# Optimization experiments

Hardware: AMD Instinct MI355X
Metric: run time of the kernel (lower is better)

## Reference

```python
import jax, jax.numpy as jnp
import numpy as np

EPS = 1e-5
OUTPUT_BINS = 1000


def _act_quant(x):
    # per-token absmax int8 quantization (BitNet b1.58)
    scale = 127.0 / jnp.clip(jnp.max(jnp.abs(x), axis=-1, keepdims=True), EPS, None)
    return jnp.clip(jnp.round(x * scale), -128.0, 127.0) / scale


def _weight_quant(w):
    # ternary absmean quantization
    scale = 1.0 / jnp.clip(jnp.mean(jnp.abs(w)), EPS, None)
    return jnp.clip(jnp.round(w * scale), -1.0, 1.0) / scale


def _ste(x, q):
    return x + jax.lax.stop_gradient(q - x)


def bitlinear(x, w):
    xq = _ste(x, _act_quant(x))
    wq = _ste(w, _weight_quant(w))
    return jnp.einsum('bi,oi->bo', xq, wq)


def layernorm(x, g, b):
    mu = jnp.mean(x, axis=-1, keepdims=True)
    var = jnp.mean(jnp.square(x - mu), axis=-1, keepdims=True)
    return (x - mu) * jax.lax.rsqrt(var + EPS) * g + b


def setup_inputs() -> dict:
    key = jax.random.key(0)
    ks = jax.random.split(key, 5)
    B, D_IN, H = 4096, 1024, 4096
    return {
        'x': jax.random.normal(ks[0], (B, D_IN), dtype=jnp.float32),
        'W0': jax.random.normal(ks[1], (H, D_IN), dtype=jnp.float32) * 0.02,
        'W1': jax.random.normal(ks[2], (H, H), dtype=jnp.float32) * 0.02,
        'W2': jax.random.normal(ks[3], (H, H), dtype=jnp.float32) * 0.02,
        'W3': jax.random.normal(ks[4], (2 * OUTPUT_BINS, H), dtype=jnp.float32) * 0.02,
        'g0': jnp.ones((H,), jnp.float32), 'b0': jnp.zeros((H,), jnp.float32),
        'g1': jnp.ones((H,), jnp.float32), 'b1': jnp.zeros((H,), jnp.float32),
        'g2': jnp.ones((H,), jnp.float32), 'b2': jnp.zeros((H,), jnp.float32),
    }


def reference(x, W0, W1, W2, W3, g0, b0, g1, b1, g2, b2):
    h = jax.nn.silu(layernorm(bitlinear(x, W0), g0, b0))
    h = jax.nn.silu(layernorm(bitlinear(h, W1), g1, b1))
    h = jax.nn.silu(layernorm(bitlinear(h, W2), g2, b2))
    out = bitlinear(h, W3)                      # [B, 2*output_bins]
    mz_logits, int_logits = jnp.split(out, 2, axis=-1)
    mz_values = jax.nn.sigmoid(mz_logits) * (OUTPUT_BINS - 1) + 1.0
    intensities = jax.nn.sigmoid(int_logits) * 100.0
    return (mz_values, intensities)
```

## Files before the change

kernel.cpp:

```cpp
#include <hip/hip_runtime.h>
#include <hip/hip_bf16.h>
#include <cstdint>
#include <cstddef>

#define EPS 1e-5f

typedef __attribute__((ext_vector_type(4))) int int32x4;

__device__ __forceinline__ float blk_sum(float v, float* s4) {
    #pragma unroll
    for (int o = 32; o; o >>= 1) v += __shfl_down(v, o, 64);
    if ((threadIdx.x & 63) == 0) s4[threadIdx.x >> 6] = v;
    __syncthreads();
    v = s4[0] + s4[1] + s4[2] + s4[3];
    __syncthreads();
    return v;
}

__device__ __forceinline__ void blk_sum2(float& a, float& b, float* s8) {
    #pragma unroll
    for (int o = 32; o; o >>= 1) {
        a += __shfl_down(a, o, 64);
        b += __shfl_down(b, o, 64);
    }
    if ((threadIdx.x & 63) == 0) {
        s8[threadIdx.x >> 6] = a;
        s8[4 + (threadIdx.x >> 6)] = b;
    }
    __syncthreads();
    a = s8[0] + s8[1] + s8[2] + s8[3];
    b = s8[4] + s8[5] + s8[6] + s8[7];
    __syncthreads();
}

__device__ __forceinline__ float blk_max(float v, float* s4) {
    #pragma unroll
    for (int o = 32; o; o >>= 1) v = fmaxf(v, __shfl_down(v, o, 64));
    if ((threadIdx.x & 63) == 0) s4[threadIdx.x >> 6] = v;
    __syncthreads();
    v = fmaxf(fmaxf(s4[0], s4[1]), fmaxf(s4[2], s4[3]));
    __syncthreads();
    return v;
}

__device__ __forceinline__ int pack4(float a, float b, float c, float d, float lo, float hi) {
    int x0 = (int)fminf(fmaxf(a, lo), hi);
    int x1 = (int)fminf(fmaxf(b, lo), hi);
    int x2 = (int)fminf(fmaxf(c, lo), hi);
    int x3 = (int)fminf(fmaxf(d, lo), hi);
    return (x0 & 255) | ((x1 & 255) << 8) | ((x2 & 255) << 16) | ((x3 & 255) << 24);
}

__device__ __forceinline__ float bflo(unsigned u) { return __uint_as_float(u << 16); }
__device__ __forceinline__ float bfhi(unsigned u) { return __uint_as_float(u & 0xffff0000u); }

__global__ __launch_bounds__(256) void absmean_all_kernel(
    const float* __restrict__ W0, const float* __restrict__ W1,
    const float* __restrict__ W2, const float* __restrict__ W3,
    float* __restrict__ part) {
    __shared__ float s4[4];
    const float* w; int sidx; unsigned rel;
    unsigned bx = blockIdx.x;
    if (bx < 1024)      { w = W0; sidx = 0; rel = bx; }
    else if (bx < 5120) { w = W1; sidx = 1; rel = bx - 1024; }
    else if (bx < 9216) { w = W2; sidx = 2; rel = bx - 5120; }
    else                { w = W3; sidx = 3; rel = bx - 9216; }
    const float4* p = (const float4*)w + (size_t)rel * 1024 + threadIdx.x;
    float4 v0 = p[0], v1 = p[256], v2 = p[512], v3 = p[768];
    float s = fabsf(v0.x) + fabsf(v0.y) + fabsf(v0.z) + fabsf(v0.w)
            + fabsf(v1.x) + fabsf(v1.y) + fabsf(v1.z) + fabsf(v1.w)
            + fabsf(v2.x) + fabsf(v2.y) + fabsf(v2.z) + fabsf(v2.w)
            + fabsf(v3.x) + fabsf(v3.y) + fabsf(v3.z) + fabsf(v3.w);
    s = blk_sum(s, s4);
    if (threadIdx.x == 0) atomicAdd(&part[(sidx * 64 + (rel & 63)) * 16], s);
}

__global__ __launch_bounds__(256) void reduce_sums_kernel(const float* __restrict__ part,
                                                          float* __restrict__ sums) {
    int w = threadIdx.x >> 6, l = threadIdx.x & 63;
    float v = part[(w * 64 + l) * 16];
    #pragma unroll
    for (int o = 32; o; o >>= 1) v += __shfl_down(v, o, 64);
    if (l == 0) sums[w] = v;
}

__global__ __launch_bounds__(256) void wquant_all_kernel(
    const float* __restrict__ W0, const float* __restrict__ W1,
    const float* __restrict__ W2, const float* __restrict__ W3,
    int* __restrict__ q0, int* __restrict__ q1, int* __restrict__ q2, int* __restrict__ q3,
    const float* __restrict__ sums) {
    const float* w; int* q; int sidx; unsigned rel; float invN; bool pad = false;
    unsigned bx = blockIdx.x;
    if (bx < 1024)      { w = W0; q = q0; sidx = 0; rel = bx;        invN = 1.f / 4194304.f; }
    else if (bx < 5120) { w = W1; q = q1; sidx = 1; rel = bx - 1024; invN = 1.f / 16777216.f; }
    else if (bx < 9216) { w = W2; q = q2; sidx = 2; rel = bx - 5120; invN = 1.f / 16777216.f; }
    else                { w = W3; q = q3; sidx = 3; rel = bx - 9216; invN = 1.f / 8192000.f;
                          pad = (rel >= 2000); }
    int4 o = {0, 0, 0, 0};
    if (!pad) {
        float mean = fmaxf(sums[sidx] * invN, EPS);
        float scale = 1.f / mean;
        const float4* p = (const float4*)w + (size_t)rel * 1024 + threadIdx.x * 4;
        float4 v0 = p[0], v1 = p[1], v2 = p[2], v3 = p[3];
        o.x = pack4(rintf(v0.x * scale), rintf(v0.y * scale), rintf(v0.z * scale), rintf(v0.w * scale), -1.f, 1.f);
        o.y = pack4(rintf(v1.x * scale), rintf(v1.y * scale), rintf(v1.z * scale), rintf(v1.w * scale), -1.f, 1.f);
        o.z = pack4(rintf(v2.x * scale), rintf(v2.y * scale), rintf(v2.z * scale), rintf(v2.w * scale), -1.f, 1.f);
        o.w = pack4(rintf(v3.x * scale), rintf(v3.y * scale), rintf(v3.z * scale), rintf(v3.w * scale), -1.f, 1.f);
    }
    ((int4*)q)[(size_t)rel * 256 + threadIdx.x] = o;
}

__global__ __launch_bounds__(256) void actquant_kernel(const float* __restrict__ x,
                                                       int* __restrict__ q,
                                                       float* __restrict__ inv_s) {
    __shared__ float s4[4];
    int row = blockIdx.x;
    const float4* xr = (const float4*)(x + (size_t)row * 1024);
    float4 v = xr[threadIdx.x];
    float m = fmaxf(fmaxf(fabsf(v.x), fabsf(v.y)), fmaxf(fabsf(v.z), fabsf(v.w)));
    m = blk_max(m, s4);
    m = fmaxf(m, EPS);
    float scale = 127.f / m;
    if (threadIdx.x == 0) inv_s[row] = m / 127.f;
    q[(size_t)row * 256 + threadIdx.x] =
        pack4(rintf(v.x * scale), rintf(v.y * scale),
              rintf(v.z * scale), rintf(v.w * scale), -128.f, 127.f);
}

__global__ __launch_bounds__(256) void ln_silu_quant_kernel(const ushort* __restrict__ h,
                                                            const float* __restrict__ g,
                                                            const float* __restrict__ b,
                                                            int* __restrict__ q,
                                                            float* __restrict__ inv_s) {
    __shared__ float s8[8];
    int row = blockIdx.x;
    int t = threadIdx.x;
    const uint4* hr = (const uint4*)(h + (size_t)row * 4096);
    uint4 p0 = hr[t * 2], p1 = hr[t * 2 + 1];
    float f[16];
    f[0] = bflo(p0.x); f[1] = bfhi(p0.x); f[2] = bflo(p0.y); f[3] = bfhi(p0.y);
    f[4] = bflo(p0.z); f[5] = bfhi(p0.z); f[6] = bflo(p0.w); f[7] = bfhi(p0.w);
    f[8] = bflo(p1.x); f[9] = bfhi(p1.x); f[10] = bflo(p1.y); f[11] = bfhi(p1.y);
    f[12] = bflo(p1.z); f[13] = bfhi(p1.z); f[14] = bflo(p1.w); f[15] = bfhi(p1.w);
    float sum = 0.f, sq = 0.f;
    #pragma unroll
    for (int i = 0; i < 16; i++) { sum += f[i]; sq += f[i] * f[i]; }
    blk_sum2(sum, sq, s8);
    float mu = sum * (1.f / 4096.f);
    float var = sq * (1.f / 4096.f) - mu * mu;
    float rs = rsqrtf(var + EPS);
    const float4* g4 = (const float4*)g;
    const float4* b4 = (const float4*)b;
    float amax = 0.f;
    #pragma unroll
    for (int i = 0; i < 4; i++) {
        float4 gg = g4[t * 4 + i];
        float4 bb = b4[t * 4 + i];
        float y0 = (f[i * 4 + 0] - mu) * rs * gg.x + bb.x;
        float y1 = (f[i * 4 + 1] - mu) * rs * gg.y + bb.y;
        float y2 = (f[i * 4 + 2] - mu) * rs * gg.z + bb.z;
        float y3 = (f[i * 4 + 3] - mu) * rs * gg.w + bb.w;
        f[i * 4 + 0] = y0 / (1.f + expf(-y0));
        f[i * 4 + 1] = y1 / (1.f + expf(-y1));
        f[i * 4 + 2] = y2 / (1.f + expf(-y2));
        f[i * 4 + 3] = y3 / (1.f + expf(-y3));
    }
    #pragma unroll
    for (int i = 0; i < 16; i++) amax = fmaxf(amax, fabsf(f[i]));
    amax = blk_max(amax, s8);
    amax = fmaxf(amax, EPS);
    float scale = 127.f / amax;
    if (t == 0) inv_s[row] = amax / 127.f;
    int4 o;
    o.x = pack4(rintf(f[0] * scale), rintf(f[1] * scale), rintf(f[2] * scale), rintf(f[3] * scale), -128.f, 127.f);
    o.y = pack4(rintf(f[4] * scale), rintf(f[5] * scale), rintf(f[6] * scale), rintf(f[7] * scale), -128.f, 127.f);
    o.z = pack4(rintf(f[8] * scale), rintf(f[9] * scale), rintf(f[10] * scale), rintf(f[11] * scale), -128.f, 127.f);
    o.w = pack4(rintf(f[12] * scale), rintf(f[13] * scale), rintf(f[14] * scale), rintf(f[15] * scale), -128.f, 127.f);
    ((int4*)((char*)q + (size_t)row * 4096))[t] = o;
}

__device__ __forceinline__ void load_lds16(const void* g, void* l) {
    __builtin_amdgcn_global_load_lds((__attribute__((address_space(1))) void*)(g),
                                     (__attribute__((address_space(3))) void*)(l), 16, 0, 0);
}

template <int MODE>
__global__ __launch_bounds__(256, 2) void gemm_i8_kernel(
    const char* __restrict__ A, const char* __restrict__ B,
    const float* __restrict__ inv_s, const float* __restrict__ wsum, float invWN,
    int K, void* __restrict__ outp) {
    __shared__ __align__(16) char lA[128 * 128];
    __shared__ __align__(16) char lB[128 * 128];
    const int t = threadIdx.x;
    const int lane = t & 63;
    const int wave = t >> 6;
    const int bm = blockIdx.y * 128, bn = blockIdx.x * 128;
    const int wr = (wave >> 1) * 64, wc = (wave & 1) * 64;

    int32x4 acc[4][4] = {};

    const int r0 = t >> 3;
    const int c0 = (t & 7) * 16;
    const int gcol = c0 ^ (16 * (r0 & 7));
    const char* gA = A + (size_t)(bm + r0) * K + gcol;
    const char* gB = B + (size_t)(bn + r0) * K + gcol;
    char* sA = lA + t * 16;
    char* sB = lB + t * 16;

    const int fr = lane & 15;
    const int fq = lane >> 4;
    const int swz = 16 * (fr & 7);

    for (int k0 = 0; k0 < K; k0 += 128) {
        #pragma unroll
        for (int j = 0; j < 4; j++)
            load_lds16(gA + (size_t)(j * 32) * K + k0, sA + j * 4096);
        #pragma unroll
        for (int j = 0; j < 4; j++)
            load_lds16(gB + (size_t)(j * 32) * K + k0, sB + j * 4096);
        __syncthreads();

        #pragma unroll
        for (int ks = 0; ks < 2; ks++) {
            const int col = (ks * 64 + fq * 16) ^ swz;
            int32x4 af[4], bf[4];
            #pragma unroll
            for (int mt = 0; mt < 4; mt++)
                af[mt] = *(const int32x4*)(lA + (wr + mt * 16 + fr) * 128 + col);
            #pragma unroll
            for (int nt = 0; nt < 4; nt++)
                bf[nt] = *(const int32x4*)(lB + (wc + nt * 16 + fr) * 128 + col);
            #pragma unroll
            for (int mt = 0; mt < 4; mt++) {
                #pragma unroll
                for (int nt = 0; nt < 4; nt++) {
                    acc[mt][nt] = __builtin_amdgcn_mfma_i32_16x16x64_i8(af[mt], bf[nt],
                                                                        acc[mt][nt], 0, 0, 0);
                }
            }
        }
        __syncthreads();
    }

    const float wmean = fmaxf(wsum[0] * invWN, EPS);
    #pragma unroll
    for (int mt = 0; mt < 4; mt++) {
        #pragma unroll
        for (int rg = 0; rg < 4; rg++) {
            int gr = bm + wr + mt * 16 + fq * 4 + rg;
            float rowscale = inv_s[gr] * wmean;
            #pragma unroll
            for (int nt = 0; nt < 4; nt++) {
                int gc = bn + wc + nt * 16 + fr;
                float v = (float)acc[mt][nt][rg] * rowscale;
                if (MODE == 0) {
                    ((__hip_bfloat16*)outp)[(size_t)gr * 4096 + gc] = __float2bfloat16(v);
                } else {
                    if (gc < 2000) {
                        float sg = 1.f / (1.f + expf(-v));
                        float* out = (float*)outp;
                        if (gc < 1000)
                            out[(size_t)gr * 1000 + gc] = sg * 999.f + 1.f;
                        else
                            out[(size_t)4096 * 1000 + (size_t)gr * 1000 + (gc - 1000)] =
                                sg * 100.f;
                    }
                }
            }
        }
    }
}

template <int MH>
__device__ __forceinline__ void mfma_quad(int32x4 (&acc)[8][4], const int32x4 (&af)[4],
                                          const int32x4 (&bf)[4]) {
    #pragma unroll
    for (int i = 0; i < 4; i++) {
        #pragma unroll
        for (int j = 0; j < 4; j++) {
            acc[MH * 4 + i][j] =
                __builtin_amdgcn_mfma_i32_16x16x64_i8(af[i], bf[j], acc[MH * 4 + i][j], 0, 0, 0);
        }
    }
}

__global__ __launch_bounds__(512, 2) void gemm_i8_pipe(
    const char* __restrict__ A, const char* __restrict__ B,
    const float* __restrict__ inv_s, const float* __restrict__ wsum, float invWN,
    int K, __hip_bfloat16* __restrict__ outp) {
    __shared__ __align__(16) char lA[4][256][64];
    __shared__ __align__(16) char lB[4][256][64];
    const int t = threadIdx.x;
    const int lane = t & 63;
    const int wave = t >> 6;

    const int nwg = gridDim.x * gridDim.y;
    const int wg0 = blockIdx.y * gridDim.x + blockIdx.x;
    const int q8 = nwg >> 3;
    const int wg = (wg0 & 7) * q8 + (wg0 >> 3);
    const int bm = (wg / gridDim.x) * 256;
    const int bn = (wg % gridDim.x) * 256;

    const int wr = (wave >> 2) * 128;
    const int wc = (wave & 3) * 64;
    const int fr = lane & 15;
    const int fq = lane >> 4;

    const int srow = t >> 2;
    const int schunk = ((t & 3) ^ ((t >> 3) & 3)) * 16;
    const char* gA = A + (size_t)(bm + srow) * K + schunk;
    const char* gB = B + (size_t)(bn + srow) * K + schunk;
    char* sAd = &lA[0][0][0] + t * 16;
    char* sBd = &lB[0][0][0] + t * 16;

    const int rchunk = (fq ^ ((fr >> 1) & 3)) * 16;
    const char* aRd = &lA[0][0][0] + (wr + fr) * 64 + rchunk;
    const char* bRd = &lB[0][0][0] + (wc + fr) * 64 + rchunk;

    int32x4 acc[8][4] = {};
    int32x4 afX[4], afY[4], bfX[4], bfY[4];
    const int NT = K >> 6;

#define STAGE_A(buf, kt) { \
    load_lds16(gA + (size_t)(kt) * 64, sAd + (buf) * 16384); \
    load_lds16(gA + (size_t)128 * K + (size_t)(kt) * 64, sAd + (buf) * 16384 + 8192); }
#define STAGE_B(buf, kt) { \
    load_lds16(gB + (size_t)(kt) * 64, sBd + (buf) * 16384); \
    load_lds16(gB + (size_t)128 * K + (size_t)(kt) * 64, sBd + (buf) * 16384 + 8192); }
#define LD_AF(dst, buf, mh) { \
    const char* p_ = aRd + (buf) * 16384 + (mh) * 4096; \
    dst[0] = *(const int32x4*)(p_); \
    dst[1] = *(const int32x4*)(p_ + 1024); \
    dst[2] = *(const int32x4*)(p_ + 2048); \
    dst[3] = *(const int32x4*)(p_ + 3072); }
#define LD_BF(dst, buf) { \
    const char* p_ = bRd + (buf) * 16384; \
    dst[0] = *(const int32x4*)(p_); \
    dst[1] = *(const int32x4*)(p_ + 1024); \
    dst[2] = *(const int32x4*)(p_ + 2048); \
    dst[3] = *(const int32x4*)(p_ + 3072); }
#define WAITL(n) { asm volatile("s_waitcnt lgkmcnt(" #n ")" ::: "memory"); \
                   __builtin_amdgcn_sched_barrier(0); }
#define WAITV(n) { asm volatile("s_waitcnt vmcnt(" #n ")" ::: "memory"); \
                   __builtin_amdgcn_sched_barrier(0); }
#define BAR() { __builtin_amdgcn_s_barrier(); __builtin_amdgcn_sched_barrier(0); }
#define MF0(afc, bfc) { __builtin_amdgcn_s_setprio(1); mfma_quad<0>(acc, afc, bfc); \
                        __builtin_amdgcn_s_setprio(0); }
#define MF1(afc, bfc) { __builtin_amdgcn_s_setprio(1); mfma_quad<1>(acc, afc, bfc); \
                        __builtin_amdgcn_s_setprio(0); }

    STAGE_A(0, 0); STAGE_B(0, 0);
    STAGE_A(1, 1); STAGE_B(1, 1);
    STAGE_A(2, 2); STAGE_B(2, 2);
    WAITV(8);
    BAR();
    LD_BF(bfX, 0); LD_AF(afX, 0, 0);

    for (int kt = 0; kt <= NT - 8; kt += 4) {
        STAGE_A(3, kt + 3); LD_AF(afY, 0, 1); WAITL(4); MF0(afX, bfX); WAITV(6); BAR();
        STAGE_B(3, kt + 3); LD_BF(bfY, 1); LD_AF(afX, 1, 0); WAITL(8); MF1(afY, bfX); BAR();
        STAGE_A(0, kt + 4); LD_AF(afY, 1, 1); WAITL(4); MF0(afX, bfY); WAITV(6); BAR();
        STAGE_B(0, kt + 4); LD_BF(bfX, 2); LD_AF(afX, 2, 0); WAITL(8); MF1(afY, bfY); BAR();
        STAGE_A(1, kt + 5); LD_AF(afY, 2, 1); WAITL(4); MF0(afX, bfX); WAITV(6); BAR();
        STAGE_B(1, kt + 5); LD_BF(bfY, 3); LD_AF(afX, 3, 0); WAITL(8); MF1(afY, bfX); BAR();
        STAGE_A(2, kt + 6); LD_AF(afY, 3, 1); WAITL(4); MF0(afX, bfY); WAITV(6); BAR();
        STAGE_B(2, kt + 6); LD_BF(bfX, 0); LD_AF(afX, 0, 0); WAITL(8); MF1(afY, bfY); BAR();
    }

    STAGE_A(3, NT - 1); LD_AF(afY, 0, 1); WAITL(4); MF0(afX, bfX); WAITV(6); BAR();
    STAGE_B(3, NT - 1); LD_BF(bfY, 1); LD_AF(afX, 1, 0); WAITL(8); MF1(afY, bfX); BAR();
    LD_AF(afY, 1, 1); WAITL(4); MF0(afX, bfY); WAITV(4); BAR();
    LD_BF(bfX, 2); LD_AF(afX, 2, 0); WAITL(8); MF1(afY, bfY); BAR();
    LD_AF(afY, 2, 1); WAITL(4); MF0(afX, bfX); WAITV(0); BAR();
    LD_BF(bfY, 3); LD_AF(afX, 3, 0); WAITL(8); MF1(afY, bfX); BAR();
    LD_AF(afY, 3, 1); WAITL(4); MF0(afX, bfY); BAR();
    WAITL(0); MF1(afY, bfY);

#undef STAGE_A
#undef STAGE_B
#undef LD_AF
#undef LD_BF
#undef WAITL
#undef WAITV
#undef BAR
#undef MF0
#undef MF1

    const float wmean = fmaxf(wsum[0] * invWN, EPS);
    #pragma unroll
    for (int mt = 0; mt < 8; mt++) {
        #pragma unroll
        for (int rg = 0; rg < 4; rg++) {
            const int gr = bm + wr + mt * 16 + fq * 4 + rg;
            const float rowscale = inv_s[gr] * wmean;
            #pragma unroll
            for (int nt = 0; nt < 4; nt++) {
                const int gc = bn + wc + nt * 16 + fr;
                outp[(size_t)gr * 4096 + gc] =
                    __float2bfloat16((float)acc[mt][nt][rg] * rowscale);
            }
        }
    }
}

extern "C" void kernel_launch(void* const* d_in, const int* in_sizes, int n_in,
                              void* d_out, int out_size, void* d_ws, size_t ws_size,
                              hipStream_t stream) {
    const float* x  = (const float*)d_in[0];
    const float* W0 = (const float*)d_in[1];
    const float* W1 = (const float*)d_in[2];
    const float* W2 = (const float*)d_in[3];
    const float* W3 = (const float*)d_in[4];
    const float* g0 = (const float*)d_in[5];
    const float* b0 = (const float*)d_in[6];
    const float* g1 = (const float*)d_in[7];
    const float* b1 = (const float*)d_in[8];
    const float* g2 = (const float*)d_in[9];
    const float* b2 = (const float*)d_in[10];
    float* out = (float*)d_out;

    char* ws = (char*)d_ws;
    size_t off = 0;
    auto alloc = [&](size_t bytes) -> char* {
        char* p = ws + off;
        off = (off + bytes + 255) & ~(size_t)255;
        return p;
    };
    float* part = (float*)alloc(256 * 16 * sizeof(float));
    float* sums = (float*)alloc(4 * sizeof(float));
    float* inv0 = (float*)alloc(4096 * 4);
    float* inv1 = (float*)alloc(4096 * 4);
    float* inv2 = (float*)alloc(4096 * 4);
    float* inv3 = (float*)alloc(4096 * 4);
    char* wq0 = alloc(4096ll * 1024);
    char* wq1 = alloc(4096ll * 4096);
    char* wq2 = alloc(4096ll * 4096);
    char* wq3 = alloc(2048ll * 4096);
    char* a0  = alloc(4096ll * 1024);
    char* a1  = alloc(4096ll * 4096);
    char* a2  = alloc(4096ll * 4096);
    char* h   = alloc(4096ll * 4096 * 2);
    char* a3 = a1;

    hipMemsetAsync(part, 0, 256 * 16 * sizeof(float), stream);

    absmean_all_kernel<<<11216, 256, 0, stream>>>(W0, W1, W2, W3, part);
    reduce_sums_kernel<<<1, 256, 0, stream>>>(part, sums);
    actquant_kernel<<<4096, 256, 0, stream>>>(x, (int*)a0, inv0);
    wquant_all_kernel<<<11264, 256, 0, stream>>>(W0, W1, W2, W3, (int*)wq0, (int*)wq1,
                                                 (int*)wq2, (int*)wq3, sums);

    gemm_i8_pipe<<<dim3(16, 16), 512, 0, stream>>>(a0, wq0, inv0, sums + 0,
                                                   1.f / 4194304.f, 1024,
                                                   (__hip_bfloat16*)h);
    ln_silu_quant_kernel<<<4096, 256, 0, stream>>>((const ushort*)h, g0, b0, (int*)a1, inv1);

    gemm_i8_pipe<<<dim3(16, 16), 512, 0, stream>>>(a1, wq1, inv1, sums + 1,
                                                   1.f / 16777216.f, 4096,
                                                   (__hip_bfloat16*)h);
    ln_silu_quant_kernel<<<4096, 256, 0, stream>>>((const ushort*)h, g1, b1, (int*)a2, inv2);

    gemm_i8_pipe<<<dim3(16, 16), 512, 0, stream>>>(a2, wq2, inv2, sums + 2,
                                                   1.f / 16777216.f, 4096,
                                                   (__hip_bfloat16*)h);
    ln_silu_quant_kernel<<<4096, 256, 0, stream>>>((const ushort*)h, g2, b2, (int*)a3, inv3);

    gemm_i8_kernel<1><<<dim3(16, 32), 256, 0, stream>>>(a3, wq3, inv3, sums + 3,
                                                        1.f / 8192000.f, 4096, out);
}
```

Baseline: 515.4 us.

## Restructure int8 GEMM pipeline to full-tile register double buffering per k-step

Replaces the half-tile ping-pong schedule, with two barriers per k-tile, by one that loads all 8 A fragments and 4 B fragments per k-tile into double-buffered registers. Both A and B global stages are issued together, so there is one barrier per k-tile instead of two. Launch bounds drop to one workgroup per SIMD group to make room for the larger fragment register set. This cuts synchronisation overhead but lowers occupancy and makes the LDS-read and MFMA overlap coarser.

```diff
diff --git a/kernel.cpp b/kernel.cpp
--- a/kernel.cpp
+++ b/kernel.cpp
@@ -271,20 +271,19 @@
     }
 }
 
-template <int MH>
-__device__ __forceinline__ void mfma_quad(int32x4 (&acc)[8][4], const int32x4 (&af)[4],
-                                          const int32x4 (&bf)[4]) {
-    #pragma unroll
-    for (int i = 0; i < 4; i++) {
+__device__ __forceinline__ void mfma_32(int32x4 (&acc)[8][4], const int32x4 (&af)[8],
+                                        const int32x4 (&bf)[4]) {
+    #pragma unroll
+    for (int i = 0; i < 8; i++) {
         #pragma unroll
         for (int j = 0; j < 4; j++) {
-            acc[MH * 4 + i][j] =
-                __builtin_amdgcn_mfma_i32_16x16x64_i8(af[i], bf[j], acc[MH * 4 + i][j], 0, 0, 0);
+            acc[i][j] =
+                __builtin_amdgcn_mfma_i32_16x16x64_i8(af[i], bf[j], acc[i][j], 0, 0, 0);
         }
     }
 }
 
-__global__ __launch_bounds__(512, 2) void gemm_i8_pipe(
+__global__ __launch_bounds__(512, 1) void gemm_i8_pipe(
     const char* __restrict__ A, const char* __restrict__ B,
     const float* __restrict__ inv_s, const float* __restrict__ wsum, float invWN,
     int K, __hip_bfloat16* __restrict__ outp) {
@@ -318,7 +317,7 @@
     const char* bRd = &lB[0][0][0] + (wc + fr) * 64 + rchunk;
 
     int32x4 acc[8][4] = {};
-    int32x4 afX[4], afY[4], bfX[4], bfY[4];
+    int32x4 aX[8], aY[8], bX[4], bY[4];
     const int NT = K >> 6;
 
 #define STAGE_A(buf, kt) { \
@@ -327,13 +326,17 @@
 #define STAGE_B(buf, kt) { \
     load_lds16(gB + (size_t)(kt) * 64, sBd + (buf) * 16384); \
     load_lds16(gB + (size_t)128 * K + (size_t)(kt) * 64, sBd + (buf) * 16384 + 8192); }
-#define LD_AF(dst, buf, mh) { \
-    const char* p_ = aRd + (buf) * 16384 + (mh) * 4096; \
+#define LD_A8(dst, buf) { \
+    const char* p_ = aRd + (buf) * 16384; \
     dst[0] = *(const int32x4*)(p_); \
     dst[1] = *(const int32x4*)(p_ + 1024); \
     dst[2] = *(const int32x4*)(p_ + 2048); \
-    dst[3] = *(const int32x4*)(p_ + 3072); }
-#define LD_BF(dst, buf) { \
+    dst[3] = *(const int32x4*)(p_ + 3072); \
+    dst[4] = *(const int32x4*)(p_ + 4096); \
+    dst[5] = *(const int32x4*)(p_ + 5120); \
+    dst[6] = *(const int32x4*)(p_ + 6144); \
+    dst[7] = *(const int32x4*)(p_ + 7168); }
+#define LD_B4(dst, buf) { \
     const char* p_ = bRd + (buf) * 16384; \
     dst[0] = *(const int32x4*)(p_); \
     dst[1] = *(const int32x4*)(p_ + 1024); \
@@ -344,47 +347,48 @@
 #define WAITV(n) { asm volatile("s_waitcnt vmcnt(" #n ")" ::: "memory"); \
                    __builtin_amdgcn_sched_barrier(0); }
 #define BAR() { __builtin_amdgcn_s_barrier(); __builtin_amdgcn_sched_barrier(0); }
-#define MF0(afc, bfc) { __builtin_amdgcn_s_setprio(1); mfma_quad<0>(acc, afc, bfc); \
-                        __builtin_amdgcn_s_setprio(0); }
-#define MF1(afc, bfc) { __builtin_amdgcn_s_setprio(1); mfma_quad<1>(acc, afc, bfc); \
-                        __builtin_amdgcn_s_setprio(0); }
+#define MF(afc, bfc) { __builtin_amdgcn_s_setprio(1); mfma_32(acc, afc, bfc); \
+                       __builtin_amdgcn_s_setprio(0); }
 
     STAGE_A(0, 0); STAGE_B(0, 0);
     STAGE_A(1, 1); STAGE_B(1, 1);
     STAGE_A(2, 2); STAGE_B(2, 2);
-    WAITV(8);
+    WAITV(4);
     BAR();
-    LD_BF(bfX, 0); LD_AF(afX, 0, 0);
+    LD_A8(aX, 0); LD_B4(bX, 0);
 
     for (int kt = 0; kt <= NT - 8; kt += 4) {
-        STAGE_A(3, kt + 3); LD_AF(afY, 0, 1); WAITL(4); MF0(afX, bfX); WAITV(6); BAR();
-        STAGE_B(3, kt + 3); LD_BF(bfY, 1); LD_AF(afX, 1, 0); WAITL(8); MF1(afY, bfX); BAR();
-        STAGE_A(0, kt + 4); LD_AF(afY, 1, 1); WAITL(4); MF0(afX, bfY); WAITV(6); BAR();
-        STAGE_B(0, kt + 4); LD_BF(bfX, 2); LD_AF(afX, 2, 0); WAITL(8); MF1(afY, bfY); BAR();
-        STAGE_A(1, kt + 5); LD_AF(afY, 2, 1); WAITL(4); MF0(afX, bfX); WAITV(6); BAR();
-        STAGE_B(1, kt + 5); LD_BF(bfY, 3); LD_AF(afX, 3, 0); WAITL(8); MF1(afY, bfX); BAR();
-        STAGE_A(2, kt + 6); LD_AF(afY, 3, 1); WAITL(4); MF0(afX, bfY); WAITV(6); BAR();
-        STAGE_B(2, kt + 6); LD_BF(bfX, 0); LD_AF(afX, 0, 0); WAITL(8); MF1(afY, bfY); BAR();
-    }
-
-    STAGE_A(3, NT - 1); LD_AF(afY, 0, 1); WAITL(4); MF0(afX, bfX); WAITV(6); BAR();
-    STAGE_B(3, NT - 1); LD_BF(bfY, 1); LD_AF(afX, 1, 0); WAITL(8); MF1(afY, bfX); BAR();
-    LD_AF(afY, 1, 1); WAITL(4); MF0(afX, bfY); WAITV(4); BAR();
-    LD_BF(bfX, 2); LD_AF(afX, 2, 0); WAITL(8); MF1(afY, bfY); BAR();
-    LD_AF(afY, 2, 1); WAITL(4); MF0(afX, bfX); WAITV(0); BAR();
-    LD_BF(bfY, 3); LD_AF(afX, 3, 0); WAITL(8); MF1(afY, bfX); BAR();
-    LD_AF(afY, 3, 1); WAITL(4); MF0(afX, bfY); BAR();
-    WAITL(0); MF1(afY, bfY);
+        STAGE_A(3, kt + 3); STAGE_B(3, kt + 3);
+        LD_A8(aY, 1); LD_B4(bY, 1);
+        WAITL(12); MF(aX, bX); WAITV(4); BAR();
+        STAGE_A(0, kt + 4); STAGE_B(0, kt + 4);
+        LD_A8(aX, 2); LD_B4(bX, 2);
+        WAITL(12); MF(aY, bY); WAITV(4); BAR();
+        STAGE_A(1, kt + 5); STAGE_B(1, kt + 5);
+        LD_A8(aY, 3); LD_B4(bY, 3);
+        WAITL(12); MF(aX, bX); WAITV(4); BAR();
+        STAGE_A(2, kt + 6); STAGE_B(2, kt + 6);
+        LD_A8(aX, 0); LD_B4(bX, 0);
+        WAITL(12); MF(aY, bY); WAITV(4); BAR();
+    }
+
+    STAGE_A(3, NT - 1); STAGE_B(3, NT - 1);
+    LD_A8(aY, 1); LD_B4(bY, 1);
+    WAITL(12); MF(aX, bX); WAITV(4); BAR();
+    LD_A8(aX, 2); LD_B4(bX, 2);
+    WAITL(12); MF(aY, bY); WAITV(0); BAR();
+    LD_A8(aY, 3); LD_B4(bY, 3);
+    WAITL(12); MF(aX, bX);
+    WAITL(0); MF(aY, bY);
 
 #undef STAGE_A
 #undef STAGE_B
-#undef LD_AF
-#undef LD_BF
+#undef LD_A8
+#undef LD_B4
 #undef WAITL
 #undef WAITV
 #undef BAR
-#undef MF0
-#undef MF1
+#undef MF
 
     const float wmean = fmaxf(wsum[0] * invWN, EPS);
     #pragma unroll
```

Result: slower. 551.8 us (+7.1%).

## Fuse prep kernels and replace final GEMM with pipelined 128x256 tile kernel

Applied to the files above, without the earlier changes.

The activation quantization of x now runs inside the weight absmean kernel as extra blocks. The standalone sum-reduction kernel is removed, and each weight-quant block reduces the partial sums itself. The last GEMM (W3 projection) changes from a simple single-buffered 128x128 kernel to a 512-thread, 4-stage LDS-pipelined kernel. That kernel uses 128x256 tiles, swizzled LDS, block remapping and interleaved MFMA/loads. This targets launch overhead and the poorly overlapped final GEMM, at the cost of redundant per-block reductions and more LDS per block.

```diff
diff --git a/kernel.cpp b/kernel.cpp
--- a/kernel.cpp
+++ b/kernel.cpp
@@ -54,51 +54,62 @@
 __device__ __forceinline__ float bflo(unsigned u) { return __uint_as_float(u << 16); }
 __device__ __forceinline__ float bfhi(unsigned u) { return __uint_as_float(u & 0xffff0000u); }
 
-__global__ __launch_bounds__(256) void absmean_all_kernel(
+__global__ __launch_bounds__(256) void absmean_act_kernel(
     const float* __restrict__ W0, const float* __restrict__ W1,
     const float* __restrict__ W2, const float* __restrict__ W3,
-    float* __restrict__ part) {
+    const float* __restrict__ x, float* __restrict__ part,
+    int* __restrict__ q, float* __restrict__ inv_s) {
     __shared__ float s4[4];
-    const float* w; int sidx; unsigned rel;
     unsigned bx = blockIdx.x;
-    if (bx < 1024)      { w = W0; sidx = 0; rel = bx; }
-    else if (bx < 5120) { w = W1; sidx = 1; rel = bx - 1024; }
-    else if (bx < 9216) { w = W2; sidx = 2; rel = bx - 5120; }
-    else                { w = W3; sidx = 3; rel = bx - 9216; }
-    const float4* p = (const float4*)w + (size_t)rel * 1024 + threadIdx.x;
-    float4 v0 = p[0], v1 = p[256], v2 = p[512], v3 = p[768];
-    float s = fabsf(v0.x) + fabsf(v0.y) + fabsf(v0.z) + fabsf(v0.w)
-            + fabsf(v1.x) + fabsf(v1.y) + fabsf(v1.z) + fabsf(v1.w)
-            + fabsf(v2.x) + fabsf(v2.y) + fabsf(v2.z) + fabsf(v2.w)
-            + fabsf(v3.x) + fabsf(v3.y) + fabsf(v3.z) + fabsf(v3.w);
-    s = blk_sum(s, s4);
-    if (threadIdx.x == 0) atomicAdd(&part[(sidx * 64 + (rel & 63)) * 16], s);
-}
-
-__global__ __launch_bounds__(256) void reduce_sums_kernel(const float* __restrict__ part,
-                                                          float* __restrict__ sums) {
-    int w = threadIdx.x >> 6, l = threadIdx.x & 63;
-    float v = part[(w * 64 + l) * 16];
-    #pragma unroll
-    for (int o = 32; o; o >>= 1) v += __shfl_down(v, o, 64);
-    if (l == 0) sums[w] = v;
-}
-
-__global__ __launch_bounds__(256) void wquant_all_kernel(
+    if (bx < 11216) {
+        const float* w; int sidx; unsigned rel;
+        if (bx < 1024)      { w = W0; sidx = 0; rel = bx; }
+        else if (bx < 5120) { w = W1; sidx = 1; rel = bx - 1024; }
+        else if (bx < 9216) { w = W2; sidx = 2; rel = bx - 5120; }
+        else                { w = W3; sidx = 3; rel = bx - 9216; }
+        const float4* p = (const float4*)w + (size_t)rel * 1024 + threadIdx.x;
+        float4 v0 = p[0], v1 = p[256], v2 = p[512], v3 = p[768];
+        float s = fabsf(v0.x) + fabsf(v0.y) + fabsf(v0.z) + fabsf(v0.w)
+                + fabsf(v1.x) + fabsf(v1.y) + fabsf(v1.z) + fabsf(v1.w)
+                + fabsf(v2.x) + fabsf(v2.y) + fabsf(v2.z) + fabsf(v2.w)
+                + fabsf(v3.x) + fabsf(v3.y) + fabsf(v3.z) + fabsf(v3.w);
+        s = blk_sum(s, s4);
+        if (threadIdx.x == 0) atomicAdd(&part[(sidx * 64 + (rel & 63)) * 16], s);
+    } else {
+        int row = bx - 11216;
+        const float4* xr = (const float4*)(x + (size_t)row * 1024);
+        float4 v = xr[threadIdx.x];
+        float m = fmaxf(fmaxf(fabsf(v.x), fabsf(v.y)), fmaxf(fabsf(v.z), fabsf(v.w)));
+        m = blk_max(m, s4);
+        m = fmaxf(m, EPS);
+        float scale = 127.f / m;
+        if (threadIdx.x == 0) inv_s[row] = m / 127.f;
+        q[(size_t)row * 256 + threadIdx.x] =
+            pack4(rintf(v.x * scale), rintf(v.y * scale),
+                  rintf(v.z * scale), rintf(v.w * scale), -128.f, 127.f);
+    }
+}
+
+__global__ __launch_bounds__(256) void wquant_sums_kernel(
     const float* __restrict__ W0, const float* __restrict__ W1,
     const float* __restrict__ W2, const float* __restrict__ W3,
     int* __restrict__ q0, int* __restrict__ q1, int* __restrict__ q2, int* __restrict__ q3,
-    const float* __restrict__ sums) {
+    const float* __restrict__ part, float* __restrict__ sums) {
     const float* w; int* q; int sidx; unsigned rel; float invN; bool pad = false;
+    bool writer = false;
     unsigned bx = blockIdx.x;
-    if (bx < 1024)      { w = W0; q = q0; sidx = 0; rel = bx;        invN = 1.f / 4194304.f; }
-    else if (bx < 5120) { w = W1; q = q1; sidx = 1; rel = bx - 1024; invN = 1.f / 16777216.f; }
-    else if (bx < 9216) { w = W2; q = q2; sidx = 2; rel = bx - 5120; invN = 1.f / 16777216.f; }
+    if (bx < 1024)      { w = W0; q = q0; sidx = 0; rel = bx;        invN = 1.f / 4194304.f;  writer = (bx == 0); }
+    else if (bx < 5120) { w = W1; q = q1; sidx = 1; rel = bx - 1024; invN = 1.f / 16777216.f; writer = (bx == 1024); }
+    else if (bx < 9216) { w = W2; q = q2; sidx = 2; rel = bx - 5120; invN = 1.f / 16777216.f; writer = (bx == 5120); }
     else                { w = W3; q = q3; sidx = 3; rel = bx - 9216; invN = 1.f / 8192000.f;
-                          pad = (rel >= 2000); }
+                          pad = (rel >= 2000); writer = (bx == 9216); }
+    float v = part[(sidx * 64 + (threadIdx.x & 63)) * 16];
+    #pragma unroll
+    for (int o = 1; o < 64; o <<= 1) v += __shfl_xor(v, o, 64);
+    if (writer && threadIdx.x == 0) sums[sidx] = v;
     int4 o = {0, 0, 0, 0};
     if (!pad) {
-        float mean = fmaxf(sums[sidx] * invN, EPS);
+        float mean = fmaxf(v * invN, EPS);
         float scale = 1.f / mean;
         const float4* p = (const float4*)w + (size_t)rel * 1024 + threadIdx.x * 4;
         float4 v0 = p[0], v1 = p[1], v2 = p[2], v3 = p[3];
@@ -108,23 +119,6 @@
         o.w = pack4(rintf(v3.x * scale), rintf(v3.y * scale), rintf(v3.z * scale), rintf(v3.w * scale), -1.f, 1.f);
     }
     ((int4*)q)[(size_t)rel * 256 + threadIdx.x] = o;
-}
-
-__global__ __launch_bounds__(256) void actquant_kernel(const float* __restrict__ x,
-                                                       int* __restrict__ q,
-                                                       float* __restrict__ inv_s) {
-    __shared__ float s4[4];
-    int row = blockIdx.x;
-    const float4* xr = (const float4*)(x + (size_t)row * 1024);
-    float4 v = xr[threadIdx.x];
-    float m = fmaxf(fmaxf(fabsf(v.x), fabsf(v.y)), fmaxf(fabsf(v.z), fabsf(v.w)));
-    m = blk_max(m, s4);
-    m = fmaxf(m, EPS);
-    float scale = 127.f / m;
-    if (threadIdx.x == 0) inv_s[row] = m / 127.f;
-    q[(size_t)row * 256 + threadIdx.x] =
-        pack4(rintf(v.x * scale), rintf(v.y * scale),
-              rintf(v.z * scale), rintf(v.w * scale), -128.f, 127.f);
 }
 
 __global__ __launch_bounds__(256) void ln_silu_quant_kernel(const ushort* __restrict__ h,
@@ -184,92 +178,11 @@
                                      (__attribute__((address_space(3))) void*)(l), 16, 0, 0);
 }
 
-template <int MODE>
-__global__ __launch_bounds__(256, 2) void gemm_i8_kernel(
-    const char* __restrict__ A, const char* __restrict__ B,
-    const float* __restrict__ inv_s, const float* __restrict__ wsum, float invWN,
-    int K, void* __restrict__ outp) {
-    __shared__ __align__(16) char lA[128 * 128];
-    __shared__ __align__(16) char lB[128 * 128];
-    const int t = threadIdx.x;
-    const int lane = t & 63;
-    const int wave = t >> 6;
-    const int bm = blockIdx.y * 128, bn = blockIdx.x * 128;
-    const int wr = (wave >> 1) * 64, wc = (wave & 1) * 64;
-
-    int32x4 acc[4][4] = {};
-
-    const int r0 = t >> 3;
-    const int c0 = (t & 7) * 16;
-    const int gcol = c0 ^ (16 * (r0 & 7));
-    const char* gA = A + (size_t)(bm + r0) * K + gcol;
-    const char* gB = B + (size_t)(bn + r0) * K + gcol;
-    char* sA = lA + t * 16;
-    char* sB = lB + t * 16;
-
-    const int fr = lane & 15;
-    const int fq = lane >> 4;
-    const int swz = 16 * (fr & 7);
-
-    for (int k0 = 0; k0 < K; k0 += 128) {
-        #pragma unroll
-        for (int j = 0; j < 4; j++)
-            load_lds16(gA + (size_t)(j * 32) * K + k0, sA + j * 4096);
-        #pragma unroll
-        for (int j = 0; j < 4; j++)
-            load_lds16(gB + (size_t)(j * 32) * K + k0, sB + j * 4096);
-        __syncthreads();
-
-        #pragma unroll
-        for (int ks = 0; ks < 2; ks++) {
-            const int col = (ks * 64 + fq * 16) ^ swz;
-            int32x4 af[4], bf[4];
-            #pragma unroll
-            for (int mt = 0; mt < 4; mt++)
-                af[mt] = *(const int32x4*)(lA + (wr + mt * 16 + fr) * 128 + col);
-            #pragma unroll
-            for (int nt = 0; nt < 4; nt++)
-                bf[nt] = *(const int32x4*)(lB + (wc + nt * 16 + fr) * 128 + col);
-            #pragma unroll
-            for (int mt = 0; mt < 4; mt++) {
-                #pragma unroll
-                for (int nt = 0; nt < 4; nt++) {
-                    acc[mt][nt] = __builtin_amdgcn_mfma_i32_16x16x64_i8(af[mt], bf[nt],
-                                                                        acc[mt][nt], 0, 0, 0);
-                }
-            }
-        }
-        __syncthreads();
-    }
-
-    const float wmean = fmaxf(wsum[0] * invWN, EPS);
-    #pragma unroll
-    for (int mt = 0; mt < 4; mt++) {
-        #pragma unroll
-        for (int rg = 0; rg < 4; rg++) {
-            int gr = bm + wr + mt * 16 + fq * 4 + rg;
-            float rowscale = inv_s[gr] * wmean;
-            #pragma unroll
-            for (int nt = 0; nt < 4; nt++) {
-                int gc = bn + wc + nt * 16 + fr;
-                float v = (float)acc[mt][nt][rg] * rowscale;
-                if (MODE == 0) {
-                    ((__hip_bfloat16*)outp)[(size_t)gr * 4096 + gc] = __float2bfloat16(v);
-                } else {
-                    if (gc < 2000) {
-                        float sg = 1.f / (1.f + expf(-v));
-                        float* out = (float*)outp;
-                        if (gc < 1000)
-                            out[(size_t)gr * 1000 + gc] = sg * 999.f + 1.f;
-                        else
-                            out[(size_t)4096 * 1000 + (size_t)gr * 1000 + (gc - 1000)] =
-                                sg * 100.f;
-                    }
-                }
-            }
-        }
-    }
-}
+#define WAITL(n) { asm volatile("s_waitcnt lgkmcnt(" #n ")" ::: "memory"); \
+                   __builtin_amdgcn_sched_barrier(0); }
+#define WAITV(n) { asm volatile("s_waitcnt vmcnt(" #n ")" ::: "memory"); \
+                   __builtin_amdgcn_sched_barrier(0); }
+#define BAR() { __builtin_amdgcn_s_barrier(); __builtin_amdgcn_sched_barrier(0); }
 
 template <int MH>
 __device__ __forceinline__ void mfma_quad(int32x4 (&acc)[8][4], const int32x4 (&af)[4],
@@ -339,11 +252,6 @@
     dst[1] = *(const int32x4*)(p_ + 1024); \
     dst[2] = *(const int32x4*)(p_ + 2048); \
     dst[3] = *(const int32x4*)(p_ + 3072); }
-#define WAITL(n) { asm volatile("s_waitcnt lgkmcnt(" #n ")" ::: "memory"); \
-                   __builtin_amdgcn_sched_barrier(0); }
-#define WAITV(n) { asm volatile("s_waitcnt vmcnt(" #n ")" ::: "memory"); \
-                   __builtin_amdgcn_sched_barrier(0); }
-#define BAR() { __builtin_amdgcn_s_barrier(); __builtin_amdgcn_sched_barrier(0); }
 #define MF0(afc, bfc) { __builtin_amdgcn_s_setprio(1); mfma_quad<0>(acc, afc, bfc); \
                         __builtin_amdgcn_s_setprio(0); }
 #define MF1(afc, bfc) { __builtin_amdgcn_s_setprio(1); mfma_quad<1>(acc, afc, bfc); \
@@ -380,9 +288,6 @@
 #undef STAGE_B
 #undef LD_AF
 #undef LD_BF
-#undef WAITL
-#undef WAITV
-#undef BAR
 #undef MF0
 #undef MF1
 
@@ -402,6 +307,131 @@
         }
     }
 }
+
+__device__ __forceinline__ void mfma_16x(int32x4 (&acc)[4][4], const int32x4 (&af)[4],
+                                         const int32x4 (&bf)[4]) {
+    #pragma unroll
+    for (int i = 0; i < 4; i++) {
+        #pragma unroll
+        for (int j = 0; j < 4; j++) {
+            acc[i][j] =
+                __builtin_amdgcn_mfma_i32_16x16x64_i8(af[i], bf[j], acc[i][j], 0, 0, 0);
+        }
+    }
+}
+
+__global__ __launch_bounds__(512, 2) void gemm_i8_g3(
+    const char* __restrict__ A, const char* __restrict__ B,
+    const float* __restrict__ inv_s, const float* __restrict__ wsum, float invWN,
+    int K, float* __restrict__ out) {
+    __shared__ __align__(16) char lA[4][128][64];
+    __shared__ __align__(16) char lB[4][256][64];
+    const int t = threadIdx.x;
+    const int lane = t & 63;
+    const int wave = t >> 6;
+
+    const int nwg = gridDim.x * gridDim.y;
+    const int wg0 = blockIdx.y * gridDim.x + blockIdx.x;
+    const int q8 = nwg >> 3;
+    const int wg = (wg0 & 7) * q8 + (wg0 >> 3);
+    const int bm = (wg / gridDim.x) * 128;
+    const int bn = (wg % gridDim.x) * 256;
+
+    const int wr = (wave >> 2) * 64;
+    const int wc = (wave & 3) * 64;
+    const int fr = lane & 15;
+    const int fq = lane >> 4;
+
+    const int srow = t >> 2;
+    const int schunk = ((t & 3) ^ ((t >> 3) & 3)) * 16;
+    const char* gA = A + (size_t)(bm + srow) * K + schunk;
+    const char* gB = B + (size_t)(bn + srow) * K + schunk;
+    char* sAd = &lA[0][0][0] + t * 16;
+    char* sBd = &lB[0][0][0] + t * 16;
+
+    const int rchunk = (fq ^ ((fr >> 1) & 3)) * 16;
+    const char* aRd = &lA[0][0][0] + (wr + fr) * 64 + rchunk;
+    const char* bRd = &lB[0][0][0] + (wc + fr) * 64 + rchunk;
+
+    int32x4 acc[4][4] = {};
+    int32x4 aX[4], aY[4], bX[4], bY[4];
+    const int NT = K >> 6;
+
+#define STAGE3(buf, kt) { \
+    load_lds16(gA + (size_t)(kt) * 64, sAd + (buf) * 8192); \
+    load_lds16(gB + (size_t)(kt) * 64, sBd + (buf) * 16384); \
+    load_lds16(gB + (size_t)128 * K + (size_t)(kt) * 64, sBd + (buf) * 16384 + 8192); }
+#define LD_A4(dst, buf) { \
+    const char* p_ = aRd + (buf) * 8192; \
+    dst[0] = *(const int32x4*)(p_); \
+    dst[1] = *(const int32x4*)(p_ + 1024); \
+    dst[2] = *(const int32x4*)(p_ + 2048); \
+    dst[3] = *(const int32x4*)(p_ + 3072); }
+#define LD_B4(dst, buf) { \
+    const char* p_ = bRd + (buf) * 16384; \
+    dst[0] = *(const int32x4*)(p_); \
+    dst[1] = *(const int32x4*)(p_ + 1024); \
+    dst[2] = *(const int32x4*)(p_ + 2048); \
+    dst[3] = *(const int32x4*)(p_ + 3072); }
+#define MFG(afc, bfc) { __builtin_amdgcn_s_setprio(1); mfma_16x(acc, afc, bfc); \
+                        __builtin_amdgcn_s_setprio(0); }
+
+    STAGE3(0, 0); STAGE3(1, 1); STAGE3(2, 2);
+    WAITV(3);
+    BAR();
+    LD_A4(aX, 0); LD_B4(bX, 0);
+
+    for (int kt = 0; kt <= NT - 8; kt += 4) {
+        STAGE3(3, kt + 3); LD_A4(aY, 1); LD_B4(bY, 1);
+        WAITL(8); MFG(aX, bX); WAITV(3); BAR();
+        STAGE3(0, kt + 4); LD_A4(aX, 2); LD_B4(bX, 2);
+        WAITL(8); MFG(aY, bY); WAITV(3); BAR();
+        STAGE3(1, kt + 5); LD_A4(aY, 3); LD_B4(bY, 3);
+        WAITL(8); MFG(aX, bX); WAITV(3); BAR();
+        STAGE3(2, kt + 6); LD_A4(aX, 0); LD_B4(bX, 0);
+        WAITL(8); MFG(aY, bY); WAITV(3); BAR();
+    }
+
+    STAGE3(3, NT - 1); LD_A4(aY, 1); LD_B4(bY, 1);
+    WAITL(8); MFG(aX, bX); WAITV(3); BAR();
+    LD_A4(aX, 2); LD_B4(bX, 2);
+    WAITL(8); MFG(aY, bY); WAITV(0); BAR();
+    LD_A4(aY, 3); LD_B4(bY, 3);
+    WAITL(8); MFG(aX, bX);
+    WAITL(0); MFG(aY, bY);
+
+#undef STAGE3
+#undef LD_A4
+#undef LD_B4
+#undef MFG
+
+    const float wmean = fmaxf(wsum[0] * invWN, EPS);
+    #pragma unroll
+    for (int mt = 0; mt < 4; mt++) {
+        #pragma unroll
+        for (int rg = 0; rg < 4; rg++) {
+            const int gr = bm + wr + mt * 16 + fq * 4 + rg;
+            const float rowscale = inv_s[gr] * wmean;
+            #pragma unroll
+            for (int nt = 0; nt < 4; nt++) {
+                const int gc = bn + wc + nt * 16 + fr;
+                if (gc < 2000) {
+                    float v = (float)acc[mt][nt][rg] * rowscale;
+                    float sg = 1.f / (1.f + expf(-v));
+                    if (gc < 1000)
+                        out[(size_t)gr * 1000 + gc] = sg * 999.f + 1.f;
+                    else
+                        out[(size_t)4096 * 1000 + (size_t)gr * 1000 + (gc - 1000)] =
+                            sg * 100.f;
+                }
+            }
+        }
+    }
+}
+
+#undef WAITL
+#undef WAITV
+#undef BAR
 
 extern "C" void kernel_launch(void* const* d_in, const int* in_sizes, int n_in,
                               void* d_out, int out_size, void* d_ws, size_t ws_size,
@@ -444,11 +474,10 @@
 
     hipMemsetAsync(part, 0, 256 * 16 * sizeof(float), stream);
 
-    absmean_all_kernel<<<11216, 256, 0, stream>>>(W0, W1, W2, W3, part);
-    reduce_sums_kernel<<<1, 256, 0, stream>>>(part, sums);
-    actquant_kernel<<<4096, 256, 0, stream>>>(x, (int*)a0, inv0);
-    wquant_all_kernel<<<11264, 256, 0, stream>>>(W0, W1, W2, W3, (int*)wq0, (int*)wq1,
-                                                 (int*)wq2, (int*)wq3, sums);
+    absmean_act_kernel<<<15312, 256, 0, stream>>>(W0, W1, W2, W3, x, part,
+                                                  (int*)a0, inv0);
+    wquant_sums_kernel<<<11264, 256, 0, stream>>>(W0, W1, W2, W3, (int*)wq0, (int*)wq1,
+                                                  (int*)wq2, (int*)wq3, part, sums);
 
     gemm_i8_pipe<<<dim3(16, 16), 512, 0, stream>>>(a0, wq0, inv0, sums + 0,
                                                    1.f / 4194304.f, 1024,
@@ -465,6 +494,6 @@
                                                    (__hip_bfloat16*)h);
     ln_silu_quant_kernel<<<4096, 256, 0, stream>>>((const ushort*)h, g2, b2, (int*)a3, inv3);
 
-    gemm_i8_kernel<1><<<dim3(16, 32), 256, 0, stream>>>(a3, wq3, inv3, sums + 3,
-                                                        1.f / 8192000.f, 4096, out);
-}
+    gemm_i8_g3<<<dim3(8, 32), 512, 0, stream>>>(a3, wq3, inv3, sums + 3,
+                                                1.f / 8192000.f, 4096, out);
+}
```

After: 521.2 us. Within noise of the previous version (+1.1%).
